# Optimization experiments

Measured on AMD Instinct MI355X. Metric: run time of the kernel, lower is better.

Reference implementation:

```python
import jax, jax.numpy as jnp
import numpy as np

GROUPS = 32
EPS = 1e-5


def group_norm(x, gamma, beta):
    # x: [B,H,W,C], channels_last, groups over channel dim (Keras GroupNormalization default)
    B, H, W, C = x.shape
    xg = x.reshape(B, H, W, GROUPS, C // GROUPS)
    mean = xg.mean(axis=(1, 2, 4), keepdims=True)
    var = xg.var(axis=(1, 2, 4), keepdims=True)
    xn = ((xg - mean) * jax.lax.rsqrt(var + EPS)).reshape(B, H, W, C)
    return xn * gamma + beta


def conv1x1(x, w, b):
    # 1x1 conv == per-pixel dense: [B,H,W,C] x [C,D] -> [B,H,W,D]
    return jnp.einsum('bhwc,cd->bhwd', x, w) + b


def setup_inputs() -> dict:
    key = jax.random.key(0)
    ks = jax.random.split(key, 10)
    C = 512
    s = 1.0 / np.sqrt(C)
    inp = {
        'x': jax.random.normal(ks[0], (2, 64, 64, C), dtype=jnp.float32),
        'gamma': jnp.ones((C,), jnp.float32),
        'beta': jnp.zeros((C,), jnp.float32),
        'wq': jax.random.normal(ks[1], (C, C), jnp.float32) * s,
        'bq': jnp.zeros((C,), jnp.float32),
        'wk': jax.random.normal(ks[2], (C, C), jnp.float32) * s,
        'bk': jnp.zeros((C,), jnp.float32),
        'wv': jax.random.normal(ks[3], (C, C), jnp.float32) * s,
        'bv': jnp.zeros((C,), jnp.float32),
        'wp': jax.random.normal(ks[4], (C, C), jnp.float32) * s,
        'bp': jnp.zeros((C,), jnp.float32),
    }
    return inp


def reference(x, gamma, beta, wq, bq, wk, bk, wv, bv, wp, bp):
    B, H, W, C = x.shape
    N = H * W
    xn = group_norm(x, gamma, beta)
    q = conv1x1(xn, wq, bq).reshape(B, N, C)
    k = conv1x1(xn, wk, bk).reshape(B, N, C)
    v = conv1x1(xn, wv, bv).reshape(B, N, C)
    scale = 1.0 / jnp.sqrt(jnp.asarray(C, x.dtype))
    scores = jnp.einsum('bnc,bmc->bnm', q, k) * scale  # [B,N,N]
    attn = jax.nn.softmax(scores, axis=-1)
    out = jnp.einsum('bnm,bmc->bnc', attn, v).reshape(B, H, W, C)
    return conv1x1(out, wp, bp) + x
```

## Files before the change

### kernel.cpp

```cpp
#include <hip/hip_runtime.h>
#include <hip/hip_fp16.h>

typedef _Float16 half_t;
typedef _Float16 half8 __attribute__((ext_vector_type(8)));
typedef float floatx4 __attribute__((ext_vector_type(4)));

static constexpr int BATCH = 2;
static constexpr int NSP = 4096;
static constexpr int CH = 512;
static constexpr int NQKV = 3 * CH;
static constexpr int KSPLIT = 4;

static constexpr size_t OFF_STATS = 0;
static constexpr size_t OFF_ROWSUM = 512;
static constexpr size_t OFF_PST = 33280;
static constexpr size_t OFF_WQKV = 196608;
static constexpr size_t WQKV_BYTES = (size_t)NQKV * CH * 2;
static constexpr size_t OFF_WP = OFF_WQKV + WQKV_BYTES;
static constexpr size_t WP_BYTES = (size_t)CH * CH * 2;
static constexpr size_t OFF_XN = OFF_WP + WP_BYTES;
static constexpr size_t XN_BYTES = (size_t)BATCH * NSP * CH * 2;
static constexpr size_t OFF_QKV = OFF_XN + XN_BYTES;
static constexpr size_t QKV_BYTES = (size_t)BATCH * NSP * NQKV * 2;
static constexpr size_t OFF_VT = OFF_QKV + QKV_BYTES;
static constexpr size_t OFF_AO = OFF_VT + XN_BYTES;
static constexpr size_t OFF_S = OFF_AO + XN_BYTES;
static constexpr size_t S_BYTES_1 = (size_t)NSP * NSP * 2;
static constexpr size_t OFF_PART = OFF_XN;

__device__ __forceinline__ void gld16(void* lds, const void* g) {
  __builtin_amdgcn_global_load_lds(
      (__attribute__((address_space(1))) void*)(g),
      (__attribute__((address_space(3))) void*)(lds),
      16, 0, 0);
}

#define VMCNT(n) asm volatile("s_waitcnt vmcnt(" #n ")" ::: "memory")
#define LGKM0()                                         \
  do {                                                  \
    asm volatile("s_waitcnt lgkmcnt(0)" ::: "memory");  \
    __builtin_amdgcn_sched_barrier(0);                  \
  } while (0)

__global__ __launch_bounds__(256) void prep(
    const float* __restrict__ x, float* __restrict__ pst,
    const float* __restrict__ w0, const float* __restrict__ w1,
    const float* __restrict__ w2, const float* __restrict__ w3,
    half_t* __restrict__ o0, half_t* __restrict__ o1,
    half_t* __restrict__ o2, half_t* __restrict__ o3) {
  __shared__ float gs[32], gs2[32];
  __shared__ float tw[32][33];
  const int bid = (int)blockIdx.x;
  const int tid = (int)threadIdx.x;
  if (bid < 512) {
    const int b = bid >> 8;
    const int chunk = bid & 255;
    int g = ((tid * 4) & (CH - 1)) >> 4;
    const float* base = x + (long)b * NSP * CH + (long)chunk * 16 * CH + tid * 4;
    float s = 0.f, s2 = 0.f;
#pragma unroll
    for (int it = 0; it < 8; ++it) {
      floatx4 v = *(const floatx4*)(base + (long)it * 1024);
#pragma unroll
      for (int r = 0; r < 4; ++r) { s += v[r]; s2 += v[r] * v[r]; }
    }
    if (tid < 32) { gs[tid] = 0.f; gs2[tid] = 0.f; }
    __syncthreads();
    atomicAdd(&gs[g], s);
    atomicAdd(&gs2[g], s2);
    __syncthreads();
    if (tid < 32) {
      long idx = ((long)(b * 256 + chunk) * 32 + tid) * 2;
      pst[idx] = gs[tid];
      pst[idx + 1] = gs2[tid];
    }
  } else {
    const int t = bid - 512;
    const int wz = t >> 8;
    const int r = t & 255;
    const float* w; half_t* o;
    switch (wz) {
      case 0: w = w0; o = o0; break;
      case 1: w = w1; o = o1; break;
      case 2: w = w2; o = o2; break;
      default: w = w3; o = o3; break;
    }
    int d0 = (r & 15) * 32, c0 = (r >> 4) * 32;
    int tx = tid & 31, ty = tid >> 5;
#pragma unroll
    for (int i = 0; i < 4; ++i)
      tw[ty + i * 8][tx] = w[(long)(c0 + ty + i * 8) * CH + d0 + tx];
    __syncthreads();
#pragma unroll
    for (int i = 0; i < 4; ++i) {
      int d = ty + i * 8;
      o[(long)(d0 + d) * CH + c0 + tx] = (half_t)tw[tx][d];
    }
  }
}

__global__ __launch_bounds__(256) void gn_finalize(const float* __restrict__ pst,
                                                   float* __restrict__ st,
                                                   float* __restrict__ rowsum) {
  int tid = (int)threadIdx.x;
  int bg = tid & 63;
  int p = tid >> 6;
  int b = bg >> 5, g = bg & 31;
  float s = 0.f, s2 = 0.f;
  for (int j = 0; j < 64; ++j) {
    int chunk = p * 64 + j;
    long idx = ((long)(b * 256 + chunk) * 32 + g) * 2;
    s += pst[idx];
    s2 += pst[idx + 1];
  }
  __shared__ float rs[64][4], rs2[64][4];
  rs[bg][p] = s;
  rs2[bg][p] = s2;
  __syncthreads();
  if (tid < 64) {
    float ts = rs[tid][0] + rs[tid][1] + rs[tid][2] + rs[tid][3];
    float ts2 = rs2[tid][0] + rs2[tid][1] + rs2[tid][2] + rs2[tid][3];
    const float inv = 1.f / 65536.f;
    float mean = ts * inv;
    float var = ts2 * inv - mean * mean;
    st[tid * 2] = mean;
    st[tid * 2 + 1] = rsqrtf(var + 1e-5f);
  }
  floatx4* rz = (floatx4*)rowsum;
#pragma unroll
  for (int j = 0; j < 8; ++j)
    rz[tid + j * 256] = floatx4{0.f, 0.f, 0.f, 0.f};
}

__global__ __launch_bounds__(256) void gn_apply(const float* __restrict__ x,
                                                const float* __restrict__ st,
                                                const float* __restrict__ gamma,
                                                const float* __restrict__ beta,
                                                half_t* __restrict__ xn) {
  long i = ((long)blockIdx.x * 256 + threadIdx.x) * 8;
  int c = (int)(i & (CH - 1));
  int b = (int)(i >> 21);
  int g = c >> 4;
  float mean = st[((b << 5) + g) * 2];
  float rstd = st[((b << 5) + g) * 2 + 1];
  floatx4 a = *(const floatx4*)(x + i);
  floatx4 d = *(const floatx4*)(x + i + 4);
  half8 o;
#pragma unroll
  for (int r = 0; r < 4; ++r) {
    o[r]     = (half_t)((a[r] - mean) * rstd * gamma[c + r] + beta[c + r]);
    o[r + 4] = (half_t)((d[r] - mean) * rstd * gamma[c + r + 4] + beta[c + r + 4]);
  }
  *(half8*)(xn + i) = o;
}

__global__ __launch_bounds__(256) void transpose_v(const half_t* __restrict__ v,
                                                   half_t* __restrict__ vt,
                                                   const half_t* __restrict__ qkv) {
  __shared__ half_t t[32][33];
  const int tid = (int)threadIdx.x;
  const int lin = (int)(blockIdx.x + gridDim.x * (blockIdx.y + gridDim.y * blockIdx.z));
  const int xcd = lin & 7;
  const int wi = lin >> 3;

  {
    int row = (xcd & 3) * 1024 + wi * 2 + (tid >> 7);
    const long* p = (const long*)((const char*)qkv + (long)row * 3072 + (tid & 127) * 8);
    long qa = *p;
    int krow = (xcd >> 2) * 2048 + wi * 4 + (tid >> 6);
    const floatx4* kp = (const floatx4*)((const char*)qkv + 1024 + (long)krow * 3072 + (tid & 63) * 16);
    floatx4 ka = *kp;
    asm volatile("" :: "v"((int)qa), "v"((int)(qa >> 32)),
                 "v"(ka[0]), "v"(ka[1]), "v"(ka[2]), "v"(ka[3]));
  }

  int b = blockIdx.z;
  int d0 = blockIdx.x * 32, n0 = blockIdx.y * 32;
  int tx = tid & 31, ty = tid >> 5;
  const half_t* vb = v + (long)b * NSP * NQKV;
  half_t* ob = vt + (long)b * NSP * CH;
#pragma unroll
  for (int i = 0; i < 4; ++i)
    t[ty + i * 8][tx] = vb[(long)(n0 + ty + i * 8) * NQKV + d0 + tx];
  __syncthreads();
#pragma unroll
  for (int i = 0; i < 4; ++i) {
    int d = ty + i * 8;
    ob[(long)(d0 + d) * NSP + n0 + tx] = t[tx][d];
  }
}

template <int BM, int BN, int BK, int EPI, int SWZ, int KSP, typename OutT>
__global__ __launch_bounds__(256) void gemm_nt(
    const half_t* __restrict__ X, const half_t* __restrict__ Y,
    OutT* __restrict__ Co, const float* __restrict__ b0,
    const float* __restrict__ b1, const float* __restrict__ b2,
    const float* __restrict__ resid, float* __restrict__ rowsum,
    int M, int N, int K, int ldx, int ldy, int ldc,
    long xbs, long ybs, long cbs, float scale) {
  constexpr int SM = BM / 32;
  constexpr int SN = BN / 32;
  constexpr int ROWS = BM + BN;
  constexpr int CPR = BK / 8;
  constexpr int RPW = 64 / CPR;
  constexpr int ROUNDS = (ROWS * BK * 2) / 4096;
  constexpr int KSTEPS = BK / 32;
  static_assert(BM % (4 * RPW) == 0, "no As/Bs straddle within a round");
  __shared__ __align__(16) half_t Sh[ROWS * BK];

  const int zb = blockIdx.z / KSP;
  const int ks = blockIdx.z % KSP;
  int bx, by;
  if (SWZ == 1) {
    int lin = (int)(blockIdx.x + gridDim.x * blockIdx.y);
    int wmt = 256 / (int)gridDim.x;
    by = wmt * (lin >> 8) + ((lin & 255) % wmt);
    bx = (lin & 255) / wmt;
  } else if (SWZ == 2) {
    by = blockIdx.x;
    bx = blockIdx.y;
  } else {
    bx = blockIdx.x;
    by = blockIdx.y;
  }

  const half_t* Xb = X + (long)zb * xbs + (long)ks * K;
  const half_t* Yb = Y + (long)zb * ybs + (long)ks * K;
  OutT* Cb = Co + (long)blockIdx.z * cbs;

  const int m0 = by * BM;
  const int n0 = bx * BN;
  const int tid = (int)threadIdx.x;
  const int wave = tid >> 6;
  const int lane = tid & 63;
  const int quad = lane >> 4;
  const int l16 = lane & 15;
  const int wm = wave >> 1;
  const int wn = wave & 1;

  floatx4 acc[SM][SN] = {};

  const int srow = lane / CPR;
  const int schunk = lane % CPR;
  const char* Xc = (const char*)Xb;

  int soff[ROUNDS];
#pragma unroll
  for (int r = 0; r < ROUNDS; ++r) {
    int row = r * (4 * RPW) + wave * RPW + srow;
    int gchunk = schunk ^ (row & (CPR - 1));
    const char* p = (row < BM)
        ? (const char*)(Xb + (long)(m0 + row) * ldx)
        : (const char*)(Yb + (long)(n0 + row - BM) * ldy);
    soff[r] = (int)(p + gchunk * 16 - Xc);
  }

  int offA[SM], offB[SN];
#pragma unroll
  for (int i = 0; i < SM; ++i) {
    int m = wm * (BM / 2) + i * 16 + l16;
    int cc = quad ^ (m & (CPR - 1));
    offA[i] = (m * BK + cc * 8) * 2;
  }
#pragma unroll
  for (int j = 0; j < SN; ++j) {
    int n = wn * (BN / 2) + j * 16 + l16;
    int cc = quad ^ (n & (CPR - 1));
    offB[j] = (BM * BK + n * BK + cc * 8) * 2;
  }

  for (int k0 = 0; k0 < K; k0 += BK) {
#pragma unroll
    for (int r = 0; r < ROUNDS; ++r) {
      gld16((char*)Sh + (r * 4 + wave) * 1024, Xc + (long)soff[r]);
      soff[r] += BK * 2;
    }
    __syncthreads();

#pragma unroll
    for (int kk = 0; kk < KSTEPS; ++kk) {
      const int kx = kk << 6;
      half8 af[SM], bf[SN];
#pragma unroll
      for (int i = 0; i < SM; ++i)
        af[i] = *(const half8*)((const char*)Sh + (offA[i] ^ kx));
#pragma unroll
      for (int j = 0; j < SN; ++j)
        bf[j] = *(const half8*)((const char*)Sh + (offB[j] ^ kx));
#pragma unroll
      for (int i = 0; i < SM; ++i)
#pragma unroll
        for (int j = 0; j < SN; ++j)
          acc[i][j] = __builtin_amdgcn_mfma_f32_16x16x32_f16(af[i], bf[j], acc[i][j], 0, 0, 0);
    }
    __syncthreads();
  }

#pragma unroll
  for (int i = 0; i < SM; ++i) {
    int gmb = m0 + wm * (BM / 2) + i * 16 + quad * 4;
#pragma unroll
    for (int j = 0; j < SN; ++j) {
      int gn = n0 + wn * (BN / 2) + j * 16 + l16;
      float bias = 0.f, sc = 1.f;
      if (EPI == 1) {
        if (gn < CH) { bias = b0[gn]; sc = scale; }
        else if (gn < 2 * CH) { bias = b1[gn - CH]; }
        else { bias = b2[gn - 2 * CH]; }
      } else if (EPI == 2) {
        bias = b0[gn];
      }
#pragma unroll
      for (int r = 0; r < 4; ++r) {
        long idx = (long)(gmb + r) * ldc + gn;
        float v = acc[i][j][r];
        if (EPI == 1) v = (v + bias) * sc;
        if (EPI == 2) v = v + bias + resid[idx];
        Cb[idx] = (OutT)v;
      }
    }
  }
}

template <int EPI, int KSP, int SW, typename OutT>
__global__ __launch_bounds__(512, 2) void gemm8p(
    const half_t* __restrict__ X, const half_t* __restrict__ Y,
    OutT* __restrict__ Co, float* __restrict__ rowsum,
    int K, int ldx, int ldy, int ldc, long xbs, long ybs, long cbs) {
  __shared__ __align__(16) char smem[131072];
  int by, bx, zb, ks;
  if (SW == 1) {
    const int lin = (int)(blockIdx.x + (blockIdx.y << 4));
    const int xcd = lin & 7;
    const int k2 = lin >> 3;
    by = (xcd & 3) * 4 + (k2 & 3);
    bx = (xcd >> 2) * 8 + (k2 >> 2);
    zb = (int)blockIdx.z / KSP;
    ks = (int)blockIdx.z % KSP;
  } else if (SW == 2) {
    const int xcd = (int)blockIdx.x & 7;
    const int s = (int)blockIdx.x >> 3;
    const int c = xcd * 2 + (s >> 4);
    by = s & 15;
    bx = c & 1;
    ks = (c >> 1) & 3;
    zb = c >> 3;
  } else {
    by = (int)blockIdx.x;
    bx = (int)blockIdx.y;
    zb = (int)blockIdx.z / KSP;
    ks = (int)blockIdx.z % KSP;
  }
  const int m0 = by * 256;
  const int n0 = bx * 256;
  const int tid = (int)threadIdx.x;
  const int w = tid >> 6;
  const int l = tid & 63;
  const int quad = l >> 4;
  const int l16 = l & 15;
  const int wm = w >> 2;
  const int wn = w & 3;

  const half_t* Xb = X + (long)zb * xbs + (long)ks * K;
  const half_t* Yb = Y + (long)zb * ybs + (long)ks * K;
  OutT* Cb = Co + ((long)(zb * KSP + ks)) * cbs;
  const char* Xc = (const char*)Xb;

  int soff[8];
  {
    const int lr = l >> 3;
    const int g = (l & 7) ^ (lr & 7);
#pragma unroll
    for (int r = 0; r < 8; ++r) {
      const int R = (r * 8 + w) * 8 + lr;
      const char* p = (R < 256)
          ? (const char*)(Xb + (long)(m0 + R) * ldx)
          : (const char*)(Yb + (long)(n0 + R - 256) * ldy);
      soff[r] = (int)(p + g * 16 - Xc);
    }
  }

  int offA[8], offB[4];
#pragma unroll
  for (int i = 0; i < 8; ++i) {
    const int m = wm * 128 + i * 16 + l16;
    offA[i] = m * 128 + ((quad ^ (m & 7)) << 4);
  }
#pragma unroll
  for (int j = 0; j < 4; ++j) {
    const int n = wn * 64 + j * 16 + l16;
    offB[j] = 32768 + n * 128 + ((quad ^ (n & 7)) << 4);
  }

  floatx4 acc[8][4] = {};

#pragma unroll
  for (int r = 0; r < 8; ++r) {
    gld16(smem + (r * 8 + w) * 1024, Xc + (long)soff[r]);
    soff[r] += 128;
  }
  {
    constexpr int pr[6] = {4, 5, 6, 7, 0, 2};
#pragma unroll
    for (int t = 0; t < 6; ++t) {
      gld16(smem + 65536 + (pr[t] * 8 + w) * 1024, Xc + (long)soff[pr[t]]);
      soff[pr[t]] += 128;
    }
  }
  VMCNT(6);
  __builtin_amdgcn_s_barrier();

  const int NI = K >> 7;
  half8 bf[4][2];
  for (int it = 0; it < NI; ++it) {
    const bool last = (it == NI - 1);
    constexpr int sr0[8] = {1, 4, 6, 0, 1, 4, 6, 0};
    constexpr int sr1[8] = {3, 5, 7, 2, 3, 5, 7, 2};
    constexpr int spar[8] = {1, 0, 0, 0, 0, 1, 1, 1};
    constexpr int hoist[8] = {1, 1, 1, 0, 1, 0, 1, 0};
    half8 af[2][2];
#pragma unroll
    for (int ph = 0; ph < 8; ++ph) {
      const int q = ph & 3;
      const char* bb = smem + (ph >> 2) * 65536;
      if (q == 0) {
#pragma unroll
        for (int j = 0; j < 4; ++j)
#pragma unroll
          for (int kk = 0; kk < 2; ++kk)
            bf[j][kk] = *(const half8*)(bb + (offB[j] ^ (kk << 6)));
#pragma unroll
        for (int i2 = 0; i2 < 2; ++i2)
#pragma unroll
          for (int kk = 0; kk < 2; ++kk)
            af[i2][kk] = *(const half8*)(bb + (offA[i2] ^ (kk << 6)));
      } else if (ph == 6) {
#pragma unroll
        for (int i2 = 0; i2 < 2; ++i2)
#pragma unroll
          for (int kk = 0; kk < 2; ++kk)
            af[i2][kk] = *(const half8*)(bb + (offA[q * 2 + i2] ^ (kk << 6)));
      }
      if (ph == 0 || !last) {
        const int r0 = sr0[ph], r1 = sr1[ph];
        char* db = smem + spar[ph] * 65536;
        gld16(db + (r0 * 8 + w) * 1024, Xc + (long)soff[r0]);
        soff[r0] += 128;
        gld16(db + (r1 * 8 + w) * 1024, Xc + (long)soff[r1]);
        soff[r1] += 128;
      }
      LGKM0();
      __builtin_amdgcn_s_setprio(1);
#pragma unroll
      for (int i2 = 0; i2 < 2; ++i2)
#pragma unroll
        for (int j = 0; j < 4; ++j)
#pragma unroll
          for (int kk = 0; kk < 2; ++kk)
            acc[q * 2 + i2][j] = __builtin_amdgcn_mfma_f32_16x16x32_f16(
                af[i2][kk], bf[j][kk], acc[q * 2 + i2][j], 0, 0, 0);
      __builtin_amdgcn_s_setprio(0);
      if (ph == 3) {
        if (last) { VMCNT(2); } else { VMCNT(8); }
      } else if (ph == 5) {
        if (last) { VMCNT(0); } else { VMCNT(10); }
      }
      if (hoist[ph]) {
        const int np = ph + 1;
        const int nq = np & 3;
        const char* nb = smem + ((np >> 2) & 1) * 65536;
#pragma unroll
        for (int i2 = 0; i2 < 2; ++i2)
#pragma unroll
          for (int kk = 0; kk < 2; ++kk)
            af[i2][kk] = *(const half8*)(nb + (offA[nq * 2 + i2] ^ (kk << 6)));
        __builtin_amdgcn_sched_barrier(0);
      }
      if (ph == 7) {
        if (!last) { VMCNT(6); }
      }
      __builtin_amdgcn_s_barrier();
    }
  }

#pragma unroll
  for (int i = 0; i < 8; ++i) {
    const int gmb = m0 + wm * 128 + i * 16 + quad * 4;
    float rs[4] = {0.f, 0.f, 0.f, 0.f};
#pragma unroll
    for (int j = 0; j < 4; ++j) {
      const int gn = n0 + wn * 64 + j * 16 + l16;
#pragma unroll
      for (int r = 0; r < 4; ++r) {
        long idx = (long)(gmb + r) * ldc + gn;
        float v = acc[i][j][r];
        if (EPI == 3) { v = __expf(v); rs[r] += v; }
        Cb[idx] = (OutT)v;
      }
    }
    if (EPI == 3) {
#pragma unroll
      for (int r = 0; r < 4; ++r) {
        float v = rs[r];
        v += __shfl_xor(v, 1);
        v += __shfl_xor(v, 2);
        v += __shfl_xor(v, 4);
        v += __shfl_xor(v, 8);
        if (l16 == 0) atomicAdd(&rowsum[(long)zb * NSP + gmb + r], v);
      }
    }
  }
}

__global__ __launch_bounds__(256) void pv_combine(const half_t* __restrict__ part,
                                                  const float* __restrict__ rowsum,
                                                  half_t* __restrict__ ao) {
  const long bNC = (long)NSP * CH;
  long i = ((long)blockIdx.x * 256 + threadIdx.x) * 8;
  int b = (int)(i >> 21);
  long inner = i & ((1L << 21) - 1);
  float inv = 1.f / rowsum[i >> 9];
  float s[8] = {};
#pragma unroll
  for (int ks = 0; ks < KSPLIT; ++ks) {
    half8 h = *(const half8*)(part + ((long)(b * KSPLIT + ks)) * bNC + inner);
#pragma unroll
    for (int r = 0; r < 8; ++r) s[r] += (float)h[r];
  }
  half8 o;
#pragma unroll
  for (int r = 0; r < 8; ++r) o[r] = (half_t)(s[r] * inv);
  *(half8*)(ao + i) = o;
}

extern "C" void kernel_launch(void* const* d_in, const int* in_sizes, int n_in,
                              void* d_out, int out_size, void* d_ws, size_t ws_size,
                              hipStream_t stream) {
  const float* x = (const float*)d_in[0];
  const float* gamma = (const float*)d_in[1];
  const float* beta = (const float*)d_in[2];
  const float* wq = (const float*)d_in[3];
  const float* bq = (const float*)d_in[4];
  const float* wk = (const float*)d_in[5];
  const float* bk = (const float*)d_in[6];
  const float* wv = (const float*)d_in[7];
  const float* bv = (const float*)d_in[8];
  const float* wp = (const float*)d_in[9];
  const float* bp = (const float*)d_in[10];
  float* out = (float*)d_out;
  char* ws = (char*)d_ws;

  float* st = (float*)(ws + OFF_STATS);
  float* rsum = (float*)(ws + OFF_ROWSUM);
  float* pst = (float*)(ws + OFF_PST);
  half_t* wqkvT = (half_t*)(ws + OFF_WQKV);
  half_t* wpT = (half_t*)(ws + OFF_WP);
  half_t* xn = (half_t*)(ws + OFF_XN);
  half_t* qkv = (half_t*)(ws + OFF_QKV);
  half_t* vt = (half_t*)(ws + OFF_VT);
  half_t* ao = (half_t*)(ws + OFF_AO);
  half_t* S = (half_t*)(ws + OFF_S);
  half_t* part = (half_t*)(ws + OFF_PART);

  half_t* q = qkv;
  half_t* k = qkv + CH;
  half_t* v = qkv + 2 * CH;

  const float scale = 0.044194173824159216f;
  const long bQKV = (long)NSP * NQKV;
  const long bNC = (long)NSP * CH;
  const long bNN = (long)NSP * NSP;

  prep<<<1536, 256, 0, stream>>>(x, pst, wq, wk, wv, wp,
      wqkvT, wqkvT + (size_t)CH * CH, wqkvT + 2 * (size_t)CH * CH, wpT);
  gn_finalize<<<1, 256, 0, stream>>>(pst, st, rsum);
  gn_apply<<<2048, 256, 0, stream>>>(x, st, gamma, beta, xn);

  gemm_nt<128, 128, 64, 1, 2, 1, half_t><<<dim3(BATCH * NSP / 128, NQKV / 128, 1), 256, 0, stream>>>(
      xn, wqkvT, qkv, bq, bk, bv, nullptr, nullptr, BATCH * NSP, NQKV, CH,
      CH, CH, NQKV, 0, 0, 0, scale);
  transpose_v<<<dim3(16, 128, BATCH), 256, 0, stream>>>(v, vt, qkv);

  bool full = ws_size >= OFF_S + 2 * S_BYTES_1;
  if (full) {
    gemm8p<3, 1, 1, half_t><<<dim3(16, 16, BATCH), 512, 0, stream>>>(
        q, k, S, rsum, CH, NQKV, NQKV, NSP, bQKV, bQKV, bNN);
    gemm8p<0, KSPLIT, 2, half_t><<<dim3(256, 1, 1), 512, 0, stream>>>(
        S, vt, part, nullptr, NSP / KSPLIT, NSP, NSP, CH, bNN, bNC, bNC);
    pv_combine<<<2048, 256, 0, stream>>>(part, rsum, ao);
  } else {
    for (int bb = 0; bb < BATCH; ++bb) {
      gemm8p<3, 1, 1, half_t><<<dim3(16, 16, 1), 512, 0, stream>>>(
          q + bb * bQKV, k + bb * bQKV, S, rsum + bb * NSP, CH,
          NQKV, NQKV, NSP, 0, 0, 0);
      gemm8p<0, KSPLIT, 0, half_t><<<dim3(NSP / 256, CH / 256, KSPLIT), 512, 0, stream>>>(
          S, vt + bb * bNC, part + (long)bb * KSPLIT * bNC, nullptr,
          NSP / KSPLIT, NSP, NSP, CH, 0, 0, bNC);
    }
    pv_combine<<<2048, 256, 0, stream>>>(part, rsum, ao);
  }
  gemm_nt<64, 64, 128, 2, 2, 1, float><<<dim3(BATCH * NSP / 64, CH / 64, 1), 256, 0, stream>>>(
      ao, wpT, out, bp, nullptr, nullptr, x, nullptr, BATCH * NSP, CH, CH,
      CH, CH, CH, 0, 0, 0, 1.f);
}
```

Before: 237.6 us.

## Compute two output tiles per QK^T block, overlapping next tile loads with epilogue

The QK^T score GEMM now has each 512-thread block compute two adjacent 256x256 output tiles in sequence. The global-to-LDS prefetch for the second tile is issued before the first tile's exp/store epilogue, so those loads overlap the epilogue. The grid shrinks from 512 to 256 blocks, with a new XCD-aware swizzle that maps tile pairs. The dummy q/k prefetch loads that transpose_v used to warm the L2 are removed. The trade-off is half as many blocks, which may reduce latency hiding and wave-level parallelism.

```diff
diff --git a/kernel.cpp b/kernel.cpp
--- a/kernel.cpp
+++ b/kernel.cpp
@@ -155,28 +155,11 @@
 }
 
 __global__ __launch_bounds__(256) void transpose_v(const half_t* __restrict__ v,
-                                                   half_t* __restrict__ vt,
-                                                   const half_t* __restrict__ qkv) {
+                                                   half_t* __restrict__ vt) {
   __shared__ half_t t[32][33];
-  const int tid = (int)threadIdx.x;
-  const int lin = (int)(blockIdx.x + gridDim.x * (blockIdx.y + gridDim.y * blockIdx.z));
-  const int xcd = lin & 7;
-  const int wi = lin >> 3;
-
-  {
-    int row = (xcd & 3) * 1024 + wi * 2 + (tid >> 7);
-    const long* p = (const long*)((const char*)qkv + (long)row * 3072 + (tid & 127) * 8);
-    long qa = *p;
-    int krow = (xcd >> 2) * 2048 + wi * 4 + (tid >> 6);
-    const floatx4* kp = (const floatx4*)((const char*)qkv + 1024 + (long)krow * 3072 + (tid & 63) * 16);
-    floatx4 ka = *kp;
-    asm volatile("" :: "v"((int)qa), "v"((int)(qa >> 32)),
-                 "v"(ka[0]), "v"(ka[1]), "v"(ka[2]), "v"(ka[3]));
-  }
-
   int b = blockIdx.z;
   int d0 = blockIdx.x * 32, n0 = blockIdx.y * 32;
-  int tx = tid & 31, ty = tid >> 5;
+  int tx = threadIdx.x & 31, ty = threadIdx.x >> 5;
   const half_t* vb = v + (long)b * NSP * NQKV;
   half_t* ob = vt + (long)b * NSP * CH;
 #pragma unroll
@@ -322,7 +305,7 @@
   }
 }
 
-template <int EPI, int KSP, int SW, typename OutT>
+template <int EPI, int KSP, int SW, int TT, typename OutT>
 __global__ __launch_bounds__(512, 2) void gemm8p(
     const half_t* __restrict__ X, const half_t* __restrict__ Y,
     OutT* __restrict__ Co, float* __restrict__ rowsum,
@@ -345,6 +328,13 @@
     bx = c & 1;
     ks = (c >> 1) & 3;
     zb = c >> 3;
+  } else if (SW == 3) {
+    const int xcd = (int)blockIdx.x & 7;
+    const int k2 = (int)blockIdx.x >> 3;
+    by = (xcd & 3) * 4 + (k2 & 3);
+    bx = ((xcd >> 2) * 4 + (k2 >> 2)) * 2;
+    zb = (int)blockIdx.z;
+    ks = 0;
   } else {
     by = (int)blockIdx.x;
     bx = (int)blockIdx.y;
@@ -352,7 +342,7 @@
     ks = (int)blockIdx.z % KSP;
   }
   const int m0 = by * 256;
-  const int n0 = bx * 256;
+  int n0 = bx * 256;
   const int tid = (int)threadIdx.x;
   const int w = tid >> 6;
   const int l = tid & 63;
@@ -366,18 +356,16 @@
   OutT* Cb = Co + ((long)(zb * KSP + ks)) * cbs;
   const char* Xc = (const char*)Xb;
 
+  const int lr = l >> 3;
+  const int gsl = (l & 7) ^ (lr & 7);
   int soff[8];
-  {
-    const int lr = l >> 3;
-    const int g = (l & 7) ^ (lr & 7);
-#pragma unroll
-    for (int r = 0; r < 8; ++r) {
-      const int R = (r * 8 + w) * 8 + lr;
-      const char* p = (R < 256)
-          ? (const char*)(Xb + (long)(m0 + R) * ldx)
-          : (const char*)(Yb + (long)(n0 + R - 256) * ldy);
-      soff[r] = (int)(p + g * 16 - Xc);
-    }
+#pragma unroll
+  for (int r = 0; r < 8; ++r) {
+    const int R = (r * 8 + w) * 8 + lr;
+    const char* p = (R < 256)
+        ? (const char*)(Xb + (long)(m0 + R) * ldx)
+        : (const char*)(Yb + (long)(n0 + R - 256) * ldy);
+    soff[r] = (int)(p + gsl * 16 - Xc);
   }
 
   int offA[8], offB[4];
@@ -392,8 +380,6 @@
     offB[j] = 32768 + n * 128 + ((quad ^ (n & 7)) << 4);
   }
 
-  floatx4 acc[8][4] = {};
-
 #pragma unroll
   for (int r = 0; r < 8; ++r) {
     gld16(smem + (r * 8 + w) * 1024, Xc + (long)soff[r]);
@@ -407,108 +393,137 @@
       soff[pr[t]] += 128;
     }
   }
-  VMCNT(6);
-  __builtin_amdgcn_s_barrier();
 
   const int NI = K >> 7;
   half8 bf[4][2];
-  for (int it = 0; it < NI; ++it) {
-    const bool last = (it == NI - 1);
-    constexpr int sr0[8] = {1, 4, 6, 0, 1, 4, 6, 0};
-    constexpr int sr1[8] = {3, 5, 7, 2, 3, 5, 7, 2};
-    constexpr int spar[8] = {1, 0, 0, 0, 0, 1, 1, 1};
-    constexpr int hoist[8] = {1, 1, 1, 0, 1, 0, 1, 0};
-    half8 af[2][2];
-#pragma unroll
-    for (int ph = 0; ph < 8; ++ph) {
-      const int q = ph & 3;
-      const char* bb = smem + (ph >> 2) * 65536;
-      if (q == 0) {
-#pragma unroll
-        for (int j = 0; j < 4; ++j)
-#pragma unroll
-          for (int kk = 0; kk < 2; ++kk)
-            bf[j][kk] = *(const half8*)(bb + (offB[j] ^ (kk << 6)));
+
+  for (int tt = 0; tt < TT; ++tt) {
+    floatx4 acc[8][4] = {};
+    VMCNT(6);
+    __builtin_amdgcn_s_barrier();
+
+    for (int it = 0; it < NI; ++it) {
+      const bool last = (it == NI - 1);
+      constexpr int sr0[8] = {1, 4, 6, 0, 1, 4, 6, 0};
+      constexpr int sr1[8] = {3, 5, 7, 2, 3, 5, 7, 2};
+      constexpr int spar[8] = {1, 0, 0, 0, 0, 1, 1, 1};
+      constexpr int hoist[8] = {1, 1, 1, 0, 1, 0, 1, 0};
+      half8 af[2][2];
+#pragma unroll
+      for (int ph = 0; ph < 8; ++ph) {
+        const int q = ph & 3;
+        const char* bb = smem + (ph >> 2) * 65536;
+        if (q == 0) {
+#pragma unroll
+          for (int j = 0; j < 4; ++j)
+#pragma unroll
+            for (int kk = 0; kk < 2; ++kk)
+              bf[j][kk] = *(const half8*)(bb + (offB[j] ^ (kk << 6)));
+#pragma unroll
+          for (int i2 = 0; i2 < 2; ++i2)
+#pragma unroll
+            for (int kk = 0; kk < 2; ++kk)
+              af[i2][kk] = *(const half8*)(bb + (offA[i2] ^ (kk << 6)));
+        } else if (ph == 6) {
+#pragma unroll
+          for (int i2 = 0; i2 < 2; ++i2)
+#pragma unroll
+            for (int kk = 0; kk < 2; ++kk)
+              af[i2][kk] = *(const half8*)(bb + (offA[q * 2 + i2] ^ (kk << 6)));
+        }
+        if (ph == 0 || !last) {
+          const int r0 = sr0[ph], r1 = sr1[ph];
+          char* db = smem + spar[ph] * 65536;
+          gld16(db + (r0 * 8 + w) * 1024, Xc + (long)soff[r0]);
+          soff[r0] += 128;
+          gld16(db + (r1 * 8 + w) * 1024, Xc + (long)soff[r1]);
+          soff[r1] += 128;
+        }
+        LGKM0();
+        __builtin_amdgcn_s_setprio(1);
 #pragma unroll
         for (int i2 = 0; i2 < 2; ++i2)
 #pragma unroll
-          for (int kk = 0; kk < 2; ++kk)
-            af[i2][kk] = *(const half8*)(bb + (offA[i2] ^ (kk << 6)));
-      } else if (ph == 6) {
-#pragma unroll
-        for (int i2 = 0; i2 < 2; ++i2)
-#pragma unroll
-          for (int kk = 0; kk < 2; ++kk)
-            af[i2][kk] = *(const half8*)(bb + (offA[q * 2 + i2] ^ (kk << 6)));
-      }
-      if (ph == 0 || !last) {
-        const int r0 = sr0[ph], r1 = sr1[ph];
-        char* db = smem + spar[ph] * 65536;
-        gld16(db + (r0 * 8 + w) * 1024, Xc + (long)soff[r0]);
-        soff[r0] += 128;
-        gld16(db + (r1 * 8 + w) * 1024, Xc + (long)soff[r1]);
-        soff[r1] += 128;
-      }
-      LGKM0();
-      __builtin_amdgcn_s_setprio(1);
-#pragma unroll
-      for (int i2 = 0; i2 < 2; ++i2)
-#pragma unroll
-        for (int j = 0; j < 4; ++j)
-#pragma unroll
-          for (int kk = 0; kk < 2; ++kk)
-            acc[q * 2 + i2][j] = __builtin_amdgcn_mfma_f32_16x16x32_f16(
-                af[i2][kk], bf[j][kk], acc[q * 2 + i2][j], 0, 0, 0);
-      __builtin_amdgcn_s_setprio(0);
-      if (ph == 3) {
-        if (last) { VMCNT(2); } else { VMCNT(8); }
-      } else if (ph == 5) {
-        if (last) { VMCNT(0); } else { VMCNT(10); }
-      }
-      if (hoist[ph]) {
-        const int np = ph + 1;
-        const int nq = np & 3;
-        const char* nb = smem + ((np >> 2) & 1) * 65536;
-#pragma unroll
-        for (int i2 = 0; i2 < 2; ++i2)
-#pragma unroll
-          for (int kk = 0; kk < 2; ++kk)
-            af[i2][kk] = *(const half8*)(nb + (offA[nq * 2 + i2] ^ (kk << 6)));
-        __builtin_amdgcn_sched_barrier(0);
-      }
-      if (ph == 7) {
-        if (!last) { VMCNT(6); }
-      }
-      __builtin_amdgcn_s_barrier();
-    }
-  }
-
-#pragma unroll
-  for (int i = 0; i < 8; ++i) {
-    const int gmb = m0 + wm * 128 + i * 16 + quad * 4;
-    float rs[4] = {0.f, 0.f, 0.f, 0.f};
-#pragma unroll
-    for (int j = 0; j < 4; ++j) {
-      const int gn = n0 + wn * 64 + j * 16 + l16;
-#pragma unroll
-      for (int r = 0; r < 4; ++r) {
-        long idx = (long)(gmb + r) * ldc + gn;
-        float v = acc[i][j][r];
-        if (EPI == 3) { v = __expf(v); rs[r] += v; }
-        Cb[idx] = (OutT)v;
-      }
-    }
-    if (EPI == 3) {
-#pragma unroll
-      for (int r = 0; r < 4; ++r) {
-        float v = rs[r];
-        v += __shfl_xor(v, 1);
-        v += __shfl_xor(v, 2);
-        v += __shfl_xor(v, 4);
-        v += __shfl_xor(v, 8);
-        if (l16 == 0) atomicAdd(&rowsum[(long)zb * NSP + gmb + r], v);
-      }
-    }
+          for (int j = 0; j < 4; ++j)
+#pragma unroll
+            for (int kk = 0; kk < 2; ++kk)
+              acc[q * 2 + i2][j] = __builtin_amdgcn_mfma_f32_16x16x32_f16(
+                  af[i2][kk], bf[j][kk], acc[q * 2 + i2][j], 0, 0, 0);
+        __builtin_amdgcn_s_setprio(0);
+        if (ph == 3) {
+          if (last) { VMCNT(2); } else { VMCNT(8); }
+        } else if (ph == 5) {
+          if (last) { VMCNT(0); } else { VMCNT(10); }
+        }
+        if (hoist[ph]) {
+          const int np = ph + 1;
+          const int nq = np & 3;
+          const char* nb = smem + ((np >> 2) & 1) * 65536;
+#pragma unroll
+          for (int i2 = 0; i2 < 2; ++i2)
+#pragma unroll
+            for (int kk = 0; kk < 2; ++kk)
+              af[i2][kk] = *(const half8*)(nb + (offA[nq * 2 + i2] ^ (kk << 6)));
+          __builtin_amdgcn_sched_barrier(0);
+        }
+        if (ph == 7) {
+          if (!last) { VMCNT(6); }
+        }
+        __builtin_amdgcn_s_barrier();
+      }
+    }
+
+    if (TT == 2 && tt == 0) {
+      const int n1 = n0 + 256;
+#pragma unroll
+      for (int r = 0; r < 8; ++r) {
+        const int R = (r * 8 + w) * 8 + lr;
+        const char* p = (R < 256)
+            ? (const char*)(Xb + (long)(m0 + R) * ldx)
+            : (const char*)(Yb + (long)(n1 + R - 256) * ldy);
+        soff[r] = (int)(p + gsl * 16 - Xc);
+      }
+#pragma unroll
+      for (int r = 0; r < 8; ++r) {
+        gld16(smem + (r * 8 + w) * 1024, Xc + (long)soff[r]);
+        soff[r] += 128;
+      }
+      constexpr int pr[6] = {4, 5, 6, 7, 0, 2};
+#pragma unroll
+      for (int t = 0; t < 6; ++t) {
+        gld16(smem + 65536 + (pr[t] * 8 + w) * 1024, Xc + (long)soff[pr[t]]);
+        soff[pr[t]] += 128;
+      }
+    }
+
+#pragma unroll
+    for (int i = 0; i < 8; ++i) {
+      const int gmb = m0 + wm * 128 + i * 16 + quad * 4;
+      float rs[4] = {0.f, 0.f, 0.f, 0.f};
+#pragma unroll
+      for (int j = 0; j < 4; ++j) {
+        const int gn = n0 + wn * 64 + j * 16 + l16;
+#pragma unroll
+        for (int r = 0; r < 4; ++r) {
+          long idx = (long)(gmb + r) * ldc + gn;
+          float v = acc[i][j][r];
+          if (EPI == 3) { v = __expf(v); rs[r] += v; }
+          Cb[idx] = (OutT)v;
+        }
+      }
+      if (EPI == 3) {
+#pragma unroll
+        for (int r = 0; r < 4; ++r) {
+          float v = rs[r];
+          v += __shfl_xor(v, 1);
+          v += __shfl_xor(v, 2);
+          v += __shfl_xor(v, 4);
+          v += __shfl_xor(v, 8);
+          if (l16 == 0) atomicAdd(&rowsum[(long)zb * NSP + gmb + r], v);
+        }
+      }
+    }
+    n0 += 256;
   }
 }
 
@@ -579,21 +594,21 @@
   gemm_nt<128, 128, 64, 1, 2, 1, half_t><<<dim3(BATCH * NSP / 128, NQKV / 128, 1), 256, 0, stream>>>(
       xn, wqkvT, qkv, bq, bk, bv, nullptr, nullptr, BATCH * NSP, NQKV, CH,
       CH, CH, NQKV, 0, 0, 0, scale);
-  transpose_v<<<dim3(16, 128, BATCH), 256, 0, stream>>>(v, vt, qkv);
+  transpose_v<<<dim3(16, 128, BATCH), 256, 0, stream>>>(v, vt);
 
   bool full = ws_size >= OFF_S + 2 * S_BYTES_1;
   if (full) {
-    gemm8p<3, 1, 1, half_t><<<dim3(16, 16, BATCH), 512, 0, stream>>>(
+    gemm8p<3, 1, 3, 2, half_t><<<dim3(128, 1, BATCH), 512, 0, stream>>>(
         q, k, S, rsum, CH, NQKV, NQKV, NSP, bQKV, bQKV, bNN);
-    gemm8p<0, KSPLIT, 2, half_t><<<dim3(256, 1, 1), 512, 0, stream>>>(
+    gemm8p<0, KSPLIT, 2, 1, half_t><<<dim3(256, 1, 1), 512, 0, stream>>>(
         S, vt, part, nullptr, NSP / KSPLIT, NSP, NSP, CH, bNN, bNC, bNC);
     pv_combine<<<2048, 256, 0, stream>>>(part, rsum, ao);
   } else {
     for (int bb = 0; bb < BATCH; ++bb) {
-      gemm8p<3, 1, 1, half_t><<<dim3(16, 16, 1), 512, 0, stream>>>(
+      gemm8p<3, 1, 1, 1, half_t><<<dim3(16, 16, 1), 512, 0, stream>>>(
           q + bb * bQKV, k + bb * bQKV, S, rsum + bb * NSP, CH,
           NQKV, NQKV, NSP, 0, 0, 0);
-      gemm8p<0, KSPLIT, 0, half_t><<<dim3(NSP / 256, CH / 256, KSPLIT), 512, 0, stream>>>(
+      gemm8p<0, KSPLIT, 0, 1, half_t><<<dim3(NSP / 256, CH / 256, KSPLIT), 512, 0, stream>>>(
           S, vt + bb * bNC, part + (long)bb * KSPLIT * bNC, nullptr,
           NSP / KSPLIT, NSP, NSP, CH, 0, 0, bNC);
     }
```

After: 246.0 us. +3.5%, slower.
